# Kernel tuning notes

Measured on AMD Instinct MI355X. Metric: run time of the kernel, lower is better.

Reference implementation:

```python
import jax, jax.numpy as jnp
import numpy as np

N_NODES = 100000
N_EDGES = 400000
D_IN = 128
D_OUT = 128
BN_EPS = 1e-5


def setup_inputs() -> dict:
    key = jax.random.key(0)
    k1, k2, k3, k4, k5 = jax.random.split(key, 5)
    n_feat = jax.random.normal(k1, (N_NODES, D_IN), dtype=jnp.float32)
    edge_index = jax.random.randint(k2, (2, N_EDGES), 0, N_NODES, dtype=jnp.int32)
    edge_weight = jnp.ones((N_EDGES,), dtype=jnp.float32)
    # learned params: BatchNorm1d affine + Linear(in, out, bias=False)
    gamma = jnp.ones((D_IN,), dtype=jnp.float32) + 0.1 * jax.random.normal(k3, (D_IN,), dtype=jnp.float32)
    beta = 0.1 * jax.random.normal(k4, (D_IN,), dtype=jnp.float32)
    W = jax.random.normal(k5, (D_OUT, D_IN), dtype=jnp.float32) * (1.0 / np.sqrt(D_IN))
    return {"n_feat": n_feat, "edge_index": edge_index, "edge_weight": edge_weight,
            "gamma": gamma, "beta": beta, "W": W}


def reference(n_feat, edge_index, edge_weight, gamma, beta, W):
    # BatchNorm1d (training-mode batch stats, biased variance) -> ReLU -> Linear (no bias)
    mu = jnp.mean(n_feat, axis=0)
    var = jnp.mean(jnp.square(n_feat - mu), axis=0)
    xh = (n_feat - mu) * jax.lax.rsqrt(var + BN_EPS)
    y = jax.nn.relu(gamma * xh + beta)
    h = y @ W.T  # [N, D_OUT]
    # sparse adjacency matmul: out[row] += w * h[col]
    row, col = edge_index[0], edge_index[1]
    msgs = h[col] * edge_weight[:, None]          # gather, [E, D_OUT]
    agg = jax.ops.segment_sum(msgs, row, num_segments=N_NODES)
    return h * h + agg
```

## Files before the change

kernel.cpp:

```cpp
#include <hip/hip_runtime.h>

#define N_NODES 100000
#define N_EDGES 400000
#define D 128
#define BN_EPS 1e-5f
#define ELL_CAP 32

#define NSTAT 64
#define CS_BLOCKS 625
#define CS_ITER 20
#define FILL_BLOCKS 1563

#define WS_STATS   0
#define WS_HB      (NSTAT * 256)
#define WS_DEG2    (WS_HB + N_NODES * D / 2)
#define WS_ELL2    (WS_DEG2 + N_NODES)
#define WS_ELL2_END (WS_ELL2 + N_NODES * ELL_CAP * 2)
#define WS_WB      WS_ELL2_END
#define WS_ELL_END2 (WS_WB + 8192)
#define WS_SCALE   (NSTAT * 256)
#define WS_SHIFT   (WS_SCALE + 128)
#define WS_WT      (WS_SHIFT + 128)
#define WS_H       (WS_WT + D * D)
#define WS_DEG     (WS_H + N_NODES * D)
#define WS_ROWPTR  (WS_DEG + N_NODES)
#define WS_CURSOR  (WS_ROWPTR + N_NODES + 1)
#define WS_CSRCOL  (WS_CURSOR + N_NODES)
#define WS_CSRW    (WS_CSRCOL + N_EDGES)
#define WS_END     (WS_CSRW + N_EDGES)

typedef __attribute__((ext_vector_type(8))) short short8;
typedef __attribute__((ext_vector_type(4))) float f32x4;

static __device__ __forceinline__ unsigned short f2bf(float f) {
    union { float f; unsigned u; } v; v.f = f;
    unsigned r = v.u + 0x7FFF + ((v.u >> 16) & 1);
    return (unsigned short)(r >> 16);
}
static __device__ __forceinline__ float bf2f(unsigned short b) {
    union { unsigned u; float f; } v; v.u = ((unsigned)b) << 16;
    return v.f;
}
static __device__ __forceinline__ unsigned short f2h(float f) {
    union { _Float16 h; unsigned short u; } v; v.h = (_Float16)f;
    return v.u;
}
static __device__ __forceinline__ float h2f(unsigned short u) {
    union { unsigned short u; _Float16 h; } v; v.u = u;
    return (float)v.h;
}

__global__ __launch_bounds__(256) void fused_pre_kernel(const float* __restrict__ x,
                                                        float* __restrict__ stats,
                                                        const int* __restrict__ ei,
                                                        const float* __restrict__ ew,
                                                        int* __restrict__ deg,
                                                        int2* __restrict__ ell2,
                                                        const float* __restrict__ W,
                                                        unsigned short* __restrict__ Wb) {
    int b = blockIdx.x;
    int t = threadIdx.x;
    if (b < CS_BLOCKS) {
        int tid = b * 256 + t;
        const int NTH = CS_BLOCKS * 256;
        const float4* x4 = (const float4*)x;
        float4 v[CS_ITER];
        #pragma unroll
        for (int i = 0; i < CS_ITER; i++) v[i] = x4[tid + i * NTH];
        float4 s = {0.f, 0.f, 0.f, 0.f};
        float4 q = {0.f, 0.f, 0.f, 0.f};
        #pragma unroll
        for (int i = 0; i < CS_ITER; i++) {
            s.x += v[i].x; s.y += v[i].y; s.z += v[i].z; s.w += v[i].w;
            q.x += v[i].x * v[i].x; q.y += v[i].y * v[i].y;
            q.z += v[i].z * v[i].z; q.w += v[i].w * v[i].w;
        }
        __shared__ float4 ss[256];
        __shared__ float4 sq[256];
        ss[t] = s;
        sq[t] = q;
        __syncthreads();
        if (t < 32) {
            float4 a = ss[t];
            float4 bb = sq[t];
            for (int i = 32; i < 256; i += 32) {
                float4 t1 = ss[t + i];
                float4 t2 = sq[t + i];
                a.x += t1.x; a.y += t1.y; a.z += t1.z; a.w += t1.w;
                bb.x += t2.x; bb.y += t2.y; bb.z += t2.z; bb.w += t2.w;
            }
            float* st = stats + (b % NSTAT) * 256;
            int colb = (t * 4) & 127;
            atomicAdd(&st[colb + 0], a.x);
            atomicAdd(&st[colb + 1], a.y);
            atomicAdd(&st[colb + 2], a.z);
            atomicAdd(&st[colb + 3], a.w);
            atomicAdd(&st[128 + colb + 0], bb.x);
            atomicAdd(&st[128 + colb + 1], bb.y);
            atomicAdd(&st[128 + colb + 2], bb.z);
            atomicAdd(&st[128 + colb + 3], bb.w);
        }
    } else if (b < CS_BLOCKS + FILL_BLOCKS) {
        int e = (b - CS_BLOCKS) * 256 + t;
        if (e >= N_EDGES) return;
        int r = ei[e];
        int c = ei[N_EDGES + e];
        float w = ew[e];
        int slot = atomicAdd(&deg[r], 1);
        if (slot < ELL_CAP) ell2[r * ELL_CAP + slot] = make_int2(c, __float_as_int(w));
    } else {
        int i = (b - CS_BLOCKS - FILL_BLOCKS) * 256 + t;
        float4 v = *(const float4*)(W + i * 4);
        ushort4 o;
        o.x = f2bf(v.x); o.y = f2bf(v.y); o.z = f2bf(v.z); o.w = f2bf(v.w);
        *(ushort4*)(Wb + i * 4) = o;
    }
}

#define YPAD 136
__global__ __launch_bounds__(256, 4) void gemm_mfma6_kernel(const float* __restrict__ x,
                                                            const float* __restrict__ stats,
                                                            const float* __restrict__ gamma,
                                                            const float* __restrict__ beta,
                                                            const unsigned short* __restrict__ Wb,
                                                            unsigned short* __restrict__ hh) {
    __shared__ __align__(16) unsigned short Yl[64 * YPAD];
    __shared__ float sscale[128];
    __shared__ float sshift[128];
    int t = threadIdx.x;
    int row0 = blockIdx.x * 64;
    int lane = t & 63;
    int wave = t >> 6;
    int m16  = lane & 15;
    int quad = lane >> 4;
    int wrow0 = wave * 16;
    int c4 = (t & 31) * 4;

    float4 xv[8];
    #pragma unroll
    for (int p = 0; p < 8; p++) {
        int r = (t + p * 256) >> 5;
        int grow = row0 + r;
        int srow = grow < N_NODES ? grow : N_NODES - 1;
        xv[p] = *(const float4*)(x + (size_t)srow * D + c4);
    }
    if (t < 128) {
        float sum = 0.f, sq = 0.f;
        #pragma unroll 16
        for (int c = 0; c < NSTAT; c++) {
            sum += stats[c * 256 + t];
            sq  += stats[c * 256 + 128 + t];
        }
        float mu  = sum * (1.0f / N_NODES);
        float var = sq * (1.0f / N_NODES) - mu * mu;
        float sc  = gamma[t] * rsqrtf(var + BN_EPS);
        sscale[t] = sc;
        sshift[t] = beta[t] - mu * sc;
    }
    __syncthreads();

    float4 sc = *(const float4*)(sscale + c4);
    float4 sh = *(const float4*)(sshift + c4);
    #pragma unroll
    for (int p = 0; p < 8; p++) {
        int r = (t + p * 256) >> 5;
        ushort4 y;
        y.x = f2bf(fmaxf(fmaf(xv[p].x, sc.x, sh.x), 0.f));
        y.y = f2bf(fmaxf(fmaf(xv[p].y, sc.y, sh.y), 0.f));
        y.z = f2bf(fmaxf(fmaf(xv[p].z, sc.z, sh.z), 0.f));
        y.w = f2bf(fmaxf(fmaf(xv[p].w, sc.w, sh.w), 0.f));
        *(ushort4*)(Yl + r * YPAD + c4) = y;
    }
    __syncthreads();

    f32x4 acc[8];
    #pragma unroll
    for (int nt = 0; nt < 8; nt++) acc[nt] = (f32x4){0.f, 0.f, 0.f, 0.f};

    const unsigned short* wb = Wb + m16 * D + quad * 8;
    const unsigned short* yl = Yl + (wrow0 + m16) * YPAD + quad * 8;
    #pragma unroll
    for (int kc = 0; kc < 4; kc++) {
        short8 a = *(const short8*)(yl + kc * 32);
        #pragma unroll
        for (int nt = 0; nt < 8; nt++) {
            short8 b = *(const short8*)(wb + nt * 16 * D + kc * 32);
            acc[nt] = __builtin_amdgcn_mfma_f32_16x16x32_bf16(a, b, acc[nt], 0, 0, 0);
        }
    }

    #pragma unroll
    for (int r = 0; r < 4; r++) {
        int grow = row0 + wrow0 + quad * 4 + r;
        if (grow < N_NODES) {
            unsigned short* hrow = hh + (size_t)grow * D + m16;
            #pragma unroll
            for (int nt = 0; nt < 8; nt++) {
                hrow[nt * 16] = f2h(acc[nt][r]);
            }
        }
    }
}

__global__ __launch_bounds__(256) void gather_ell6_kernel(const int* __restrict__ deg,
                                                          const int2* __restrict__ ell2,
                                                          const unsigned short* __restrict__ hh,
                                                          float* __restrict__ out) {
    int lane = threadIdx.x & 15;
    int n = blockIdx.x * 16 + (threadIdx.x >> 4);
    if (n >= N_NODES) return;
    short8 hself = *(const short8*)(hh + (size_t)n * D + lane * 8);
    int dg = __builtin_nontemporal_load(&deg[n]);
    if (dg > ELL_CAP) dg = ELL_CAP;
    int dg16 = dg < 16 ? dg : 16;

    int2 my = make_int2(0, 0);
    if (lane < dg16) my = ell2[n * ELL_CAP + lane];

    float acc[8] = {0.f, 0.f, 0.f, 0.f, 0.f, 0.f, 0.f, 0.f};
    int s = 0;
    for (; s + 4 <= dg16; s += 4) {
        int   c0 = __shfl(my.x, s + 0, 16); float w0 = __int_as_float(__shfl(my.y, s + 0, 16));
        int   c1 = __shfl(my.x, s + 1, 16); float w1 = __int_as_float(__shfl(my.y, s + 1, 16));
        int   c2 = __shfl(my.x, s + 2, 16); float w2 = __int_as_float(__shfl(my.y, s + 2, 16));
        int   c3 = __shfl(my.x, s + 3, 16); float w3 = __int_as_float(__shfl(my.y, s + 3, 16));
        short8 v0 = *(const short8*)(hh + (size_t)c0 * D + lane * 8);
        short8 v1 = *(const short8*)(hh + (size_t)c1 * D + lane * 8);
        short8 v2 = *(const short8*)(hh + (size_t)c2 * D + lane * 8);
        short8 v3 = *(const short8*)(hh + (size_t)c3 * D + lane * 8);
        #pragma unroll
        for (int j = 0; j < 8; j++) {
            acc[j] = fmaf(w0, h2f((unsigned short)v0[j]), acc[j]);
            acc[j] = fmaf(w1, h2f((unsigned short)v1[j]), acc[j]);
            acc[j] = fmaf(w2, h2f((unsigned short)v2[j]), acc[j]);
            acc[j] = fmaf(w3, h2f((unsigned short)v3[j]), acc[j]);
        }
    }
    for (; s < dg16; s++) {
        int c = __shfl(my.x, s, 16);
        float w = __int_as_float(__shfl(my.y, s, 16));
        short8 v = *(const short8*)(hh + (size_t)c * D + lane * 8);
        #pragma unroll
        for (int j = 0; j < 8; j++) acc[j] = fmaf(w, h2f((unsigned short)v[j]), acc[j]);
    }
    for (s = 16; s < dg; s++) {
        int2 cw = ell2[n * ELL_CAP + s];
        float w = __int_as_float(cw.y);
        short8 v = *(const short8*)(hh + (size_t)cw.x * D + lane * 8);
        #pragma unroll
        for (int j = 0; j < 8; j++) acc[j] = fmaf(w, h2f((unsigned short)v[j]), acc[j]);
    }

    f32x4 a, b;
    {
        float h0 = h2f((unsigned short)hself[0]); float h1 = h2f((unsigned short)hself[1]);
        float h2 = h2f((unsigned short)hself[2]); float h3 = h2f((unsigned short)hself[3]);
        float h4 = h2f((unsigned short)hself[4]); float h5 = h2f((unsigned short)hself[5]);
        float h6 = h2f((unsigned short)hself[6]); float h7 = h2f((unsigned short)hself[7]);
        a[0] = fmaf(h0, h0, acc[0]); a[1] = fmaf(h1, h1, acc[1]);
        a[2] = fmaf(h2, h2, acc[2]); a[3] = fmaf(h3, h3, acc[3]);
        b[0] = fmaf(h4, h4, acc[4]); b[1] = fmaf(h5, h5, acc[5]);
        b[2] = fmaf(h6, h6, acc[6]); b[3] = fmaf(h7, h7, acc[7]);
    }
    float* o = out + (size_t)n * D + lane * 8;
    __builtin_nontemporal_store(a, (f32x4*)o);
    __builtin_nontemporal_store(b, (f32x4*)(o + 4));
}

__global__ __launch_bounds__(256) void colstats_kernel(const float* __restrict__ x,
                                                       float* __restrict__ stats,
                                                       int* __restrict__ deg) {
    int tid = blockIdx.x * 256 + threadIdx.x;
    if (deg && tid < N_NODES) deg[tid] = 0;
    const int NTH = CS_BLOCKS * 256;
    const float4* x4 = (const float4*)x;
    float4 v[CS_ITER];
    #pragma unroll
    for (int i = 0; i < CS_ITER; i++) v[i] = x4[tid + i * NTH];
    float4 s = {0.f, 0.f, 0.f, 0.f};
    float4 q = {0.f, 0.f, 0.f, 0.f};
    #pragma unroll
    for (int i = 0; i < CS_ITER; i++) {
        s.x += v[i].x; s.y += v[i].y; s.z += v[i].z; s.w += v[i].w;
        q.x += v[i].x * v[i].x; q.y += v[i].y * v[i].y;
        q.z += v[i].z * v[i].z; q.w += v[i].w * v[i].w;
    }
    __shared__ float4 ss[256];
    __shared__ float4 sq[256];
    ss[threadIdx.x] = s;
    sq[threadIdx.x] = q;
    __syncthreads();
    if (threadIdx.x < 32) {
        float4 a = ss[threadIdx.x];
        float4 b = sq[threadIdx.x];
        for (int i = 32; i < 256; i += 32) {
            float4 t1 = ss[threadIdx.x + i];
            float4 t2 = sq[threadIdx.x + i];
            a.x += t1.x; a.y += t1.y; a.z += t1.z; a.w += t1.w;
            b.x += t2.x; b.y += t2.y; b.z += t2.z; b.w += t2.w;
        }
        float* st = stats + (blockIdx.x % NSTAT) * 256;
        int colb = (threadIdx.x * 4) & 127;
        atomicAdd(&st[colb + 0], a.x);
        atomicAdd(&st[colb + 1], a.y);
        atomicAdd(&st[colb + 2], a.z);
        atomicAdd(&st[colb + 3], a.w);
        atomicAdd(&st[128 + colb + 0], b.x);
        atomicAdd(&st[128 + colb + 1], b.y);
        atomicAdd(&st[128 + colb + 2], b.z);
        atomicAdd(&st[128 + colb + 3], b.w);
    }
}

__global__ __launch_bounds__(128) void finalize_kernel(const float* __restrict__ stats,
                                                       const float* __restrict__ gamma,
                                                       const float* __restrict__ beta,
                                                       float* __restrict__ scale,
                                                       float* __restrict__ shift) {
    int d = threadIdx.x;
    float sum = 0.f, sq = 0.f;
    #pragma unroll 16
    for (int c = 0; c < NSTAT; c++) {
        sum += stats[c * 256 + d];
        sq  += stats[c * 256 + 128 + d];
    }
    float mu  = sum * (1.0f / N_NODES);
    float var = sq * (1.0f / N_NODES) - mu * mu;
    float sc  = gamma[d] * rsqrtf(var + BN_EPS);
    scale[d] = sc;
    shift[d] = beta[d] - mu * sc;
}

__global__ __launch_bounds__(256) void transposeW_kernel(const float* __restrict__ W,
                                                         float* __restrict__ Wt) {
    int i = blockIdx.x * blockDim.x + threadIdx.x;
    if (i < D * D) {
        int j = i >> 7;
        int k = i & 127;
        Wt[k * D + j] = W[i];
    }
}

template <int WRITE_SQ>
__global__ __launch_bounds__(256) void gemm_kernel(const float* __restrict__ x,
                                                   const float* __restrict__ scale,
                                                   const float* __restrict__ shift,
                                                   const float* __restrict__ Wt,
                                                   float* __restrict__ h,
                                                   float* __restrict__ out) {
    __shared__ float Ws[D * D];
    __shared__ float Ys[32 * D];
    int t = threadIdx.x;
    const float4* Wt4 = (const float4*)Wt;
    float4* Ws4 = (float4*)Ws;
    #pragma unroll 4
    for (int i = t; i < D * D / 4; i += 256) Ws4[i] = Wt4[i];
    int row0 = blockIdx.x * 32;
    const float4* x4 = (const float4*)(x + (size_t)row0 * D);
    float4* Ys4 = (float4*)Ys;
    #pragma unroll 2
    for (int i = t; i < 32 * D / 4; i += 256) {
        int c4 = (i & 31) * 4;
        float4 v = x4[i];
        v.x = fmaxf(fmaf(v.x, scale[c4 + 0], shift[c4 + 0]), 0.f);
        v.y = fmaxf(fmaf(v.y, scale[c4 + 1], shift[c4 + 1]), 0.f);
        v.z = fmaxf(fmaf(v.z, scale[c4 + 2], shift[c4 + 2]), 0.f);
        v.w = fmaxf(fmaf(v.w, scale[c4 + 3], shift[c4 + 3]), 0.f);
        Ys4[i] = v;
    }
    __syncthreads();
    int cg = t & 31;
    int rg = t >> 5;
    float4 acc[4] = {{0,0,0,0},{0,0,0,0},{0,0,0,0},{0,0,0,0}};
    #pragma unroll 2
    for (int k = 0; k < D; k += 4) {
        float4 w0 = *(const float4*)&Ws[(k + 0) * D + cg * 4];
        float4 w1 = *(const float4*)&Ws[(k + 1) * D + cg * 4];
        float4 w2 = *(const float4*)&Ws[(k + 2) * D + cg * 4];
        float4 w3 = *(const float4*)&Ws[(k + 3) * D + cg * 4];
        #pragma unroll
        for (int r = 0; r < 4; r++) {
            float4 y = *(const float4*)&Ys[(rg * 4 + r) * D + k];
            acc[r].x = fmaf(y.x, w0.x, fmaf(y.y, w1.x, fmaf(y.z, w2.x, fmaf(y.w, w3.x, acc[r].x))));
            acc[r].y = fmaf(y.x, w0.y, fmaf(y.y, w1.y, fmaf(y.z, w2.y, fmaf(y.w, w3.y, acc[r].y))));
            acc[r].z = fmaf(y.x, w0.z, fmaf(y.y, w1.z, fmaf(y.z, w2.z, fmaf(y.w, w3.z, acc[r].z))));
            acc[r].w = fmaf(y.x, w0.w, fmaf(y.y, w1.w, fmaf(y.z, w2.w, fmaf(y.w, w3.w, acc[r].w))));
        }
    }
    #pragma unroll
    for (int r = 0; r < 4; r++) {
        size_t row = (size_t)row0 + rg * 4 + r;
        float4 v = acc[r];
        *(float4*)&h[row * D + cg * 4] = v;
        if (WRITE_SQ) {
            float4 sqv = {v.x * v.x, v.y * v.y, v.z * v.z, v.w * v.w};
            *(float4*)&out[row * D + cg * 4] = sqv;
        }
    }
}

__global__ __launch_bounds__(256) void hist_kernel(const int* __restrict__ ei,
                                                   int* __restrict__ deg) {
    int e = blockIdx.x * 256 + threadIdx.x;
    if (e < N_EDGES) atomicAdd(&deg[ei[e]], 1);
}

__global__ __launch_bounds__(1024) void scan_kernel(const int* __restrict__ deg,
                                                    int* __restrict__ row_ptr,
                                                    int* __restrict__ cursor) {
    __shared__ int part[1024];
    int t = threadIdx.x;
    const int CHUNK = 100;
    int base = t * CHUNK;
    int s = 0;
    if (base < N_NODES) {
        for (int i = 0; i < CHUNK; i++) s += deg[base + i];
    }
    part[t] = s;
    __syncthreads();
    for (int off = 1; off < 1024; off <<= 1) {
        int v = (t >= off) ? part[t - off] : 0;
        __syncthreads();
        part[t] += v;
        __syncthreads();
    }
    int pre = (t == 0) ? 0 : part[t - 1];
    if (base < N_NODES) {
        for (int i = 0; i < CHUNK; i++) {
            row_ptr[base + i] = pre;
            cursor[base + i] = pre;
            pre += deg[base + i];
        }
    }
    if (t == 1023) row_ptr[N_NODES] = part[1023];
}

__global__ __launch_bounds__(256) void fill_kernel(const int* __restrict__ ei,
                                                   const float* __restrict__ ew,
                                                   int* __restrict__ cursor,
                                                   int* __restrict__ csr_col,
                                                   float* __restrict__ csr_w) {
    int e = blockIdx.x * 256 + threadIdx.x;
    if (e >= N_EDGES) return;
    int r = ei[e];
    int c = ei[N_EDGES + e];
    int slot = atomicAdd(&cursor[r], 1);
    csr_col[slot] = c;
    csr_w[slot] = ew[e];
}

__global__ __launch_bounds__(256) void gather_kernel(const int* __restrict__ row_ptr,
                                                     const int* __restrict__ csr_col,
                                                     const float* __restrict__ csr_w,
                                                     const float* __restrict__ h,
                                                     float* __restrict__ out) {
    int lane = threadIdx.x & 31;
    int n = blockIdx.x * 8 + (threadIdx.x >> 5);
    if (n >= N_NODES) return;
    int s0 = row_ptr[n];
    int s1 = row_ptr[n + 1];
    float4 acc = {0.f, 0.f, 0.f, 0.f};
    for (int s = s0; s < s1; s++) {
        int c = csr_col[s];
        float w = csr_w[s];
        float4 v = *(const float4*)&h[(size_t)c * D + lane * 4];
        acc.x = fmaf(w, v.x, acc.x);
        acc.y = fmaf(w, v.y, acc.y);
        acc.z = fmaf(w, v.z, acc.z);
        acc.w = fmaf(w, v.w, acc.w);
    }
    float4 hv = *(const float4*)&h[(size_t)n * D + lane * 4];
    float4 o;
    o.x = fmaf(hv.x, hv.x, acc.x);
    o.y = fmaf(hv.y, hv.y, acc.y);
    o.z = fmaf(hv.z, hv.z, acc.z);
    o.w = fmaf(hv.w, hv.w, acc.w);
    *(float4*)&out[(size_t)n * D + lane * 4] = o;
}

__global__ __launch_bounds__(256) void scatter_kernel(const int* __restrict__ ei,
                                                      const float* __restrict__ ew,
                                                      const float* __restrict__ h,
                                                      float* __restrict__ out) {
    int lane = threadIdx.x & 31;
    int e = blockIdx.x * 8 + (threadIdx.x >> 5);
    if (e >= N_EDGES) return;
    int r = ei[e];
    int c = ei[N_EDGES + e];
    float w = ew[e];
    float4 v = *(const float4*)&h[(size_t)c * D + lane * 4];
    float* o = out + (size_t)r * D + lane * 4;
    atomicAdd(o + 0, v.x * w);
    atomicAdd(o + 1, v.y * w);
    atomicAdd(o + 2, v.z * w);
    atomicAdd(o + 3, v.w * w);
}

extern "C" void kernel_launch(void* const* d_in, const int* in_sizes, int n_in,
                              void* d_out, int out_size, void* d_ws, size_t ws_size,
                              hipStream_t stream) {
    const float* n_feat = (const float*)d_in[0];
    const int*   ei     = (const int*)d_in[1];
    const float* ew     = (const float*)d_in[2];
    const float* gamma  = (const float*)d_in[3];
    const float* beta   = (const float*)d_in[4];
    const float* W      = (const float*)d_in[5];
    float* out = (float*)d_out;

    float* ws    = (float*)d_ws;
    float* stats = ws + WS_STATS;

    bool ell_ok = ws_size >= (size_t)WS_ELL_END2 * sizeof(float);
    bool csr_ok = ws_size >= (size_t)WS_END * sizeof(float);

    (void)hipMemsetAsync(stats, 0, NSTAT * 256 * sizeof(float), stream);

    if (ell_ok) {
        unsigned short* hh  = (unsigned short*)(ws + WS_HB);
        int*  deg  = (int*)ws + WS_DEG2;
        int2* ell2 = (int2*)((int*)ws + WS_ELL2);
        unsigned short* Wb = (unsigned short*)(ws + WS_WB);

        (void)hipMemsetAsync(deg, 0, N_NODES * sizeof(int), stream);
        fused_pre_kernel<<<CS_BLOCKS + FILL_BLOCKS + 16, 256, 0, stream>>>(
            n_feat, stats, ei, ew, deg, ell2, W, Wb);
        gemm_mfma6_kernel<<<(N_NODES + 63) / 64, 256, 0, stream>>>(n_feat, stats, gamma, beta, Wb, hh);
        gather_ell6_kernel<<<(N_NODES + 15) / 16, 256, 0, stream>>>(deg, ell2, hh, out);
    } else if (csr_ok) {
        float* scale = ws + WS_SCALE;
        float* shift = ws + WS_SHIFT;
        float* Wt    = ws + WS_WT;
        float* h     = ws + WS_H;
        int*   deg     = (int*)ws + WS_DEG;
        int*   row_ptr = (int*)ws + WS_ROWPTR;
        int*   cursor  = (int*)ws + WS_CURSOR;
        int*   csr_col = (int*)ws + WS_CSRCOL;
        float* csr_w   = ws + WS_CSRW;

        colstats_kernel<<<CS_BLOCKS, 256, 0, stream>>>(n_feat, stats, nullptr);
        finalize_kernel<<<1, 128, 0, stream>>>(stats, gamma, beta, scale, shift);
        transposeW_kernel<<<64, 256, 0, stream>>>(W, Wt);
        (void)hipMemsetAsync(deg, 0, N_NODES * sizeof(int), stream);
        gemm_kernel<0><<<N_NODES / 32, 256, 0, stream>>>(n_feat, scale, shift, Wt, h, out);
        hist_kernel<<<(N_EDGES + 255) / 256, 256, 0, stream>>>(ei, deg);
        scan_kernel<<<1, 1024, 0, stream>>>(deg, row_ptr, cursor);
        fill_kernel<<<(N_EDGES + 255) / 256, 256, 0, stream>>>(ei, ew, cursor, csr_col, csr_w);
        gather_kernel<<<(N_NODES + 7) / 8, 256, 0, stream>>>(row_ptr, csr_col, csr_w, h, out);
    } else {
        float* scale = ws + WS_SCALE;
        float* shift = ws + WS_SHIFT;
        float* Wt    = ws + WS_WT;
        float* h     = ws + WS_H;
        colstats_kernel<<<CS_BLOCKS, 256, 0, stream>>>(n_feat, stats, nullptr);
        finalize_kernel<<<1, 128, 0, stream>>>(stats, gamma, beta, scale, shift);
        transposeW_kernel<<<64, 256, 0, stream>>>(W, Wt);
        gemm_kernel<1><<<N_NODES / 32, 256, 0, stream>>>(n_feat, scale, shift, Wt, h, out);
        scatter_kernel<<<(N_EDGES + 7) / 8, 256, 0, stream>>>(ei, ew, h, out);
    }
}
```

Baseline: 195.9 us.

## Fuse pre, GEMM and gather stages into one cooperative persistent kernel

Replaces the two memsets and three kernel launches with a single cooperative kernel of 1024 persistent blocks. Grid-wide syncs separate zero-init, stats/ELL fill/W conversion, the MFMA GEMM, and the ELL gather. Each block recomputes the BN scale and shift itself. The GEMM and gather loops become grid-stride loops. This removes launch and memset overhead and inter-kernel gaps, at the cost of grid barriers, fixed occupancy limits, and fewer threads for the edge fill role. If the cooperative launch fails, it falls back to the old path.

```diff
diff --git a/kernel.cpp b/kernel.cpp
--- a/kernel.cpp
+++ b/kernel.cpp
@@ -1,4 +1,7 @@
 #include <hip/hip_runtime.h>
+#include <hip/hip_cooperative_groups.h>
+
+namespace cg = cooperative_groups;
 
 #define N_NODES 100000
 #define N_EDGES 400000
@@ -10,6 +13,9 @@
 #define CS_BLOCKS 625
 #define CS_ITER 20
 #define FILL_BLOCKS 1563
+#define MEGA_BLOCKS 1024
+#define FILL_ROLE_THREADS (383 * 256)
+#define N_TILES 1563
 
 #define WS_STATS   0
 #define WS_HB      (NSTAT * 256)
@@ -48,6 +54,235 @@
 static __device__ __forceinline__ float h2f(unsigned short u) {
     union { unsigned short u; _Float16 h; } v; v.u = u;
     return (float)v.h;
+}
+
+#define YPAD 136
+
+__global__ __launch_bounds__(256, 4) void mega_kernel(const float* __restrict__ x,
+                                                      float* __restrict__ stats,
+                                                      const int* __restrict__ ei,
+                                                      const float* __restrict__ ew,
+                                                      int* __restrict__ deg,
+                                                      int2* __restrict__ ell2,
+                                                      const float* __restrict__ W,
+                                                      unsigned short* __restrict__ Wb,
+                                                      const float* __restrict__ gamma,
+                                                      const float* __restrict__ beta,
+                                                      unsigned short* __restrict__ hh,
+                                                      float* __restrict__ out) {
+    cg::grid_group grid = cg::this_grid();
+    __shared__ float4 ss[256];
+    __shared__ float4 sq[256];
+    __shared__ __align__(16) unsigned short Yl[64 * YPAD];
+    __shared__ float sscale[128];
+    __shared__ float sshift[128];
+
+    int b = blockIdx.x;
+    int t = threadIdx.x;
+    int gtid = b * 256 + t;
+
+    if (gtid < NSTAT * 256) stats[gtid] = 0.f;
+    {
+        int dtid = gtid - NSTAT * 256;
+        if (dtid >= 0 && dtid < N_NODES) deg[dtid] = 0;
+    }
+    grid.sync();
+
+    if (b < CS_BLOCKS) {
+        int tid = b * 256 + t;
+        const int NTH = CS_BLOCKS * 256;
+        const float4* x4 = (const float4*)x;
+        float4 v[CS_ITER];
+        #pragma unroll
+        for (int i = 0; i < CS_ITER; i++) v[i] = x4[tid + i * NTH];
+        float4 s = {0.f, 0.f, 0.f, 0.f};
+        float4 q = {0.f, 0.f, 0.f, 0.f};
+        #pragma unroll
+        for (int i = 0; i < CS_ITER; i++) {
+            s.x += v[i].x; s.y += v[i].y; s.z += v[i].z; s.w += v[i].w;
+            q.x += v[i].x * v[i].x; q.y += v[i].y * v[i].y;
+            q.z += v[i].z * v[i].z; q.w += v[i].w * v[i].w;
+        }
+        ss[t] = s;
+        sq[t] = q;
+        __syncthreads();
+        if (t < 32) {
+            float4 a = ss[t];
+            float4 bb = sq[t];
+            for (int i = 32; i < 256; i += 32) {
+                float4 t1 = ss[t + i];
+                float4 t2 = sq[t + i];
+                a.x += t1.x; a.y += t1.y; a.z += t1.z; a.w += t1.w;
+                bb.x += t2.x; bb.y += t2.y; bb.z += t2.z; bb.w += t2.w;
+            }
+            float* st = stats + (b % NSTAT) * 256;
+            int colb = (t * 4) & 127;
+            atomicAdd(&st[colb + 0], a.x);
+            atomicAdd(&st[colb + 1], a.y);
+            atomicAdd(&st[colb + 2], a.z);
+            atomicAdd(&st[colb + 3], a.w);
+            atomicAdd(&st[128 + colb + 0], bb.x);
+            atomicAdd(&st[128 + colb + 1], bb.y);
+            atomicAdd(&st[128 + colb + 2], bb.z);
+            atomicAdd(&st[128 + colb + 3], bb.w);
+        }
+    } else if (b < CS_BLOCKS + 383) {
+        int base = (b - CS_BLOCKS) * 256 + t;
+        for (int e = base; e < N_EDGES; e += FILL_ROLE_THREADS) {
+            int r = ei[e];
+            int c = ei[N_EDGES + e];
+            float w = ew[e];
+            int slot = atomicAdd(&deg[r], 1);
+            if (slot < ELL_CAP) ell2[r * ELL_CAP + slot] = make_int2(c, __float_as_int(w));
+        }
+    } else {
+        int i = (b - CS_BLOCKS - 383) * 256 + t;
+        float4 v = *(const float4*)(W + i * 4);
+        ushort4 o;
+        o.x = f2bf(v.x); o.y = f2bf(v.y); o.z = f2bf(v.z); o.w = f2bf(v.w);
+        *(ushort4*)(Wb + i * 4) = o;
+    }
+    grid.sync();
+
+    {
+        if (t < 128) {
+            float sum = 0.f, sq2 = 0.f;
+            #pragma unroll 16
+            for (int c = 0; c < NSTAT; c++) {
+                sum += stats[c * 256 + t];
+                sq2 += stats[c * 256 + 128 + t];
+            }
+            float mu  = sum * (1.0f / N_NODES);
+            float var = sq2 * (1.0f / N_NODES) - mu * mu;
+            float sc  = gamma[t] * rsqrtf(var + BN_EPS);
+            sscale[t] = sc;
+            sshift[t] = beta[t] - mu * sc;
+        }
+        __syncthreads();
+
+        int lane = t & 63;
+        int wave = t >> 6;
+        int m16  = lane & 15;
+        int quad = lane >> 4;
+        int wrow0 = wave * 16;
+        int c4 = (t & 31) * 4;
+        float4 sc = *(const float4*)(sscale + c4);
+        float4 sh = *(const float4*)(sshift + c4);
+
+        for (int tile = b; tile < N_TILES; tile += MEGA_BLOCKS) {
+            int row0 = tile * 64;
+            float4 xv[8];
+            #pragma unroll
+            for (int p = 0; p < 8; p++) {
+                int r = (t + p * 256) >> 5;
+                int grow = row0 + r;
+                int srow = grow < N_NODES ? grow : N_NODES - 1;
+                xv[p] = *(const float4*)(x + (size_t)srow * D + c4);
+            }
+            #pragma unroll
+            for (int p = 0; p < 8; p++) {
+                int r = (t + p * 256) >> 5;
+                ushort4 y;
+                y.x = f2bf(fmaxf(fmaf(xv[p].x, sc.x, sh.x), 0.f));
+                y.y = f2bf(fmaxf(fmaf(xv[p].y, sc.y, sh.y), 0.f));
+                y.z = f2bf(fmaxf(fmaf(xv[p].z, sc.z, sh.z), 0.f));
+                y.w = f2bf(fmaxf(fmaf(xv[p].w, sc.w, sh.w), 0.f));
+                *(ushort4*)(Yl + r * YPAD + c4) = y;
+            }
+            __syncthreads();
+
+            f32x4 acc[8];
+            #pragma unroll
+            for (int nt = 0; nt < 8; nt++) acc[nt] = (f32x4){0.f, 0.f, 0.f, 0.f};
+
+            const unsigned short* wb = Wb + m16 * D + quad * 8;
+            const unsigned short* yl = Yl + (wrow0 + m16) * YPAD + quad * 8;
+            #pragma unroll
+            for (int kc = 0; kc < 4; kc++) {
+                short8 a = *(const short8*)(yl + kc * 32);
+                #pragma unroll
+                for (int nt = 0; nt < 8; nt++) {
+                    short8 bb = *(const short8*)(wb + nt * 16 * D + kc * 32);
+                    acc[nt] = __builtin_amdgcn_mfma_f32_16x16x32_bf16(a, bb, acc[nt], 0, 0, 0);
+                }
+            }
+            #pragma unroll
+            for (int r = 0; r < 4; r++) {
+                int grow = row0 + wrow0 + quad * 4 + r;
+                if (grow < N_NODES) {
+                    unsigned short* hrow = hh + (size_t)grow * D + m16;
+                    #pragma unroll
+                    for (int nt = 0; nt < 8; nt++) {
+                        hrow[nt * 16] = f2h(acc[nt][r]);
+                    }
+                }
+            }
+            __syncthreads();
+        }
+    }
+    grid.sync();
+
+    {
+        int lane = t & 15;
+        for (int n = b * 16 + (t >> 4); n < N_NODES; n += MEGA_BLOCKS * 16) {
+            short8 hself = *(const short8*)(hh + (size_t)n * D + lane * 8);
+            int dg = deg[n];
+            if (dg > ELL_CAP) dg = ELL_CAP;
+            int dg16 = dg < 16 ? dg : 16;
+
+            int2 my = make_int2(0, 0);
+            if (lane < dg16) my = ell2[n * ELL_CAP + lane];
+
+            float acc[8] = {0.f, 0.f, 0.f, 0.f, 0.f, 0.f, 0.f, 0.f};
+            int s = 0;
+            for (; s + 4 <= dg16; s += 4) {
+                int   c0 = __shfl(my.x, s + 0, 16); float w0 = __int_as_float(__shfl(my.y, s + 0, 16));
+                int   c1 = __shfl(my.x, s + 1, 16); float w1 = __int_as_float(__shfl(my.y, s + 1, 16));
+                int   c2 = __shfl(my.x, s + 2, 16); float w2 = __int_as_float(__shfl(my.y, s + 2, 16));
+                int   c3 = __shfl(my.x, s + 3, 16); float w3 = __int_as_float(__shfl(my.y, s + 3, 16));
+                short8 v0 = *(const short8*)(hh + (size_t)c0 * D + lane * 8);
+                short8 v1 = *(const short8*)(hh + (size_t)c1 * D + lane * 8);
+                short8 v2 = *(const short8*)(hh + (size_t)c2 * D + lane * 8);
+                short8 v3 = *(const short8*)(hh + (size_t)c3 * D + lane * 8);
+                #pragma unroll
+                for (int j = 0; j < 8; j++) {
+                    acc[j] = fmaf(w0, h2f((unsigned short)v0[j]), acc[j]);
+                    acc[j] = fmaf(w1, h2f((unsigned short)v1[j]), acc[j]);
+                    acc[j] = fmaf(w2, h2f((unsigned short)v2[j]), acc[j]);
+                    acc[j] = fmaf(w3, h2f((unsigned short)v3[j]), acc[j]);
+                }
+            }
+            for (; s < dg16; s++) {
+                int c = __shfl(my.x, s, 16);
+                float w = __int_as_float(__shfl(my.y, s, 16));
+                short8 v = *(const short8*)(hh + (size_t)c * D + lane * 8);
+                #pragma unroll
+                for (int j = 0; j < 8; j++) acc[j] = fmaf(w, h2f((unsigned short)v[j]), acc[j]);
+            }
+            for (s = 16; s < dg; s++) {
+                int2 cw = ell2[n * ELL_CAP + s];
+                float w = __int_as_float(cw.y);
+                short8 v = *(const short8*)(hh + (size_t)cw.x * D + lane * 8);
+                #pragma unroll
+                for (int j = 0; j < 8; j++) acc[j] = fmaf(w, h2f((unsigned short)v[j]), acc[j]);
+            }
+
+            f32x4 a2, b2;
+            {
+                float h0 = h2f((unsigned short)hself[0]); float h1 = h2f((unsigned short)hself[1]);
+                float h2 = h2f((unsigned short)hself[2]); float h3 = h2f((unsigned short)hself[3]);
+                float h4 = h2f((unsigned short)hself[4]); float h5 = h2f((unsigned short)hself[5]);
+                float h6 = h2f((unsigned short)hself[6]); float h7 = h2f((unsigned short)hself[7]);
+                a2[0] = fmaf(h0, h0, acc[0]); a2[1] = fmaf(h1, h1, acc[1]);
+                a2[2] = fmaf(h2, h2, acc[2]); a2[3] = fmaf(h3, h3, acc[3]);
+                b2[0] = fmaf(h4, h4, acc[4]); b2[1] = fmaf(h5, h5, acc[5]);
+                b2[2] = fmaf(h6, h6, acc[6]); b2[3] = fmaf(h7, h7, acc[7]);
+            }
+            float* o = out + (size_t)n * D + lane * 8;
+            __builtin_nontemporal_store(a2, (f32x4*)o);
+            __builtin_nontemporal_store(b2, (f32x4*)(o + 4));
+        }
+    }
 }
 
 __global__ __launch_bounds__(256) void fused_pre_kernel(const float* __restrict__ x,
@@ -117,7 +352,6 @@
     }
 }
 
-#define YPAD 136
 __global__ __launch_bounds__(256, 4) void gemm_mfma6_kernel(const float* __restrict__ x,
                                                             const float* __restrict__ stats,
                                                             const float* __restrict__ gamma,
@@ -188,7 +422,6 @@
             acc[nt] = __builtin_amdgcn_mfma_f32_16x16x32_bf16(a, b, acc[nt], 0, 0, 0);
         }
     }
-
     #pragma unroll
     for (int r = 0; r < 4; r++) {
         int grow = row0 + wrow0 + quad * 4 + r;
@@ -369,15 +602,15 @@
         Ys4[i] = v;
     }
     __syncthreads();
-    int cg = t & 31;
+    int cg2 = t & 31;
     int rg = t >> 5;
     float4 acc[4] = {{0,0,0,0},{0,0,0,0},{0,0,0,0},{0,0,0,0}};
     #pragma unroll 2
     for (int k = 0; k < D; k += 4) {
-        float4 w0 = *(const float4*)&Ws[(k + 0) * D + cg * 4];
-        float4 w1 = *(const float4*)&Ws[(k + 1) * D + cg * 4];
-        float4 w2 = *(const float4*)&Ws[(k + 2) * D + cg * 4];
-        float4 w3 = *(const float4*)&Ws[(k + 3) * D + cg * 4];
+        float4 w0 = *(const float4*)&Ws[(k + 0) * D + cg2 * 4];
+        float4 w1 = *(const float4*)&Ws[(k + 1) * D + cg2 * 4];
+        float4 w2 = *(const float4*)&Ws[(k + 2) * D + cg2 * 4];
+        float4 w3 = *(const float4*)&Ws[(k + 3) * D + cg2 * 4];
         #pragma unroll
         for (int r = 0; r < 4; r++) {
             float4 y = *(const float4*)&Ys[(rg * 4 + r) * D + k];
@@ -391,10 +624,10 @@
     for (int r = 0; r < 4; r++) {
         size_t row = (size_t)row0 + rg * 4 + r;
         float4 v = acc[r];
-        *(float4*)&h[row * D + cg * 4] = v;
+        *(float4*)&h[row * D + cg2 * 4] = v;
         if (WRITE_SQ) {
             float4 sqv = {v.x * v.x, v.y * v.y, v.z * v.z, v.w * v.w};
-            *(float4*)&out[row * D + cg * 4] = sqv;
+            *(float4*)&out[row * D + cg2 * 4] = sqv;
         }
     }
 }
@@ -513,19 +746,28 @@
     bool ell_ok = ws_size >= (size_t)WS_ELL_END2 * sizeof(float);
     bool csr_ok = ws_size >= (size_t)WS_END * sizeof(float);
 
-    (void)hipMemsetAsync(stats, 0, NSTAT * 256 * sizeof(float), stream);
-
     if (ell_ok) {
         unsigned short* hh  = (unsigned short*)(ws + WS_HB);
         int*  deg  = (int*)ws + WS_DEG2;
         int2* ell2 = (int2*)((int*)ws + WS_ELL2);
         unsigned short* Wb = (unsigned short*)(ws + WS_WB);
 
-        (void)hipMemsetAsync(deg, 0, N_NODES * sizeof(int), stream);
-        fused_pre_kernel<<<CS_BLOCKS + FILL_BLOCKS + 16, 256, 0, stream>>>(
-            n_feat, stats, ei, ew, deg, ell2, W, Wb);
-        gemm_mfma6_kernel<<<(N_NODES + 63) / 64, 256, 0, stream>>>(n_feat, stats, gamma, beta, Wb, hh);
-        gather_ell6_kernel<<<(N_NODES + 15) / 16, 256, 0, stream>>>(deg, ell2, hh, out);
+        void* args[] = {
+            (void*)&n_feat, (void*)&stats, (void*)&ei, (void*)&ew,
+            (void*)&deg, (void*)&ell2, (void*)&W, (void*)&Wb,
+            (void*)&gamma, (void*)&beta, (void*)&hh, (void*)&out
+        };
+        hipError_t err = hipLaunchCooperativeKernel((const void*)mega_kernel,
+                                                    dim3(MEGA_BLOCKS), dim3(256),
+                                                    args, 0, stream);
+        if (err != hipSuccess) {
+            (void)hipMemsetAsync(stats, 0, NSTAT * 256 * sizeof(float), stream);
+            (void)hipMemsetAsync(deg, 0, N_NODES * sizeof(int), stream);
+            fused_pre_kernel<<<CS_BLOCKS + FILL_BLOCKS + 16, 256, 0, stream>>>(
+                n_feat, stats, ei, ew, deg, ell2, W, Wb);
+            gemm_mfma6_kernel<<<(N_NODES + 63) / 64, 256, 0, stream>>>(n_feat, stats, gamma, beta, Wb, hh);
+            gather_ell6_kernel<<<(N_NODES + 15) / 16, 256, 0, stream>>>(deg, ell2, hh, out);
+        }
     } else if (csr_ok) {
         float* scale = ws + WS_SCALE;
         float* shift = ws + WS_SHIFT;
@@ -537,6 +779,7 @@
         int*   csr_col = (int*)ws + WS_CSRCOL;
         float* csr_w   = ws + WS_CSRW;
 
+        (void)hipMemsetAsync(stats, 0, NSTAT * 256 * sizeof(float), stream);
         colstats_kernel<<<CS_BLOCKS, 256, 0, stream>>>(n_feat, stats, nullptr);
         finalize_kernel<<<1, 128, 0, stream>>>(stats, gamma, beta, scale, shift);
         transposeW_kernel<<<64, 256, 0, stream>>>(W, Wt);
@@ -551,6 +794,7 @@
         float* shift = ws + WS_SHIFT;
         float* Wt    = ws + WS_WT;
         float* h     = ws + WS_H;
+        (void)hipMemsetAsync(stats, 0, NSTAT * 256 * sizeof(float), stream);
         colstats_kernel<<<CS_BLOCKS, 256, 0, stream>>>(n_feat, stats, nullptr);
         finalize_kernel<<<1, 128, 0, stream>>>(stats, gamma, beta, scale, shift);
         transposeW_kernel<<<64, 256, 0, stream>>>(W, Wt);
```

New measurement: 489.8 us. +150.0%, slower.
